# Performance work log

Measured on AMD Instinct MI355X. Metric: run time of the kernel, lower is better.

## Reference

```python
import jax, jax.numpy as jnp
import numpy as np

WS, SS, NH = 7, 3, 3  # window_size, shift_size, num_heads


def window_partition(x, ws):
    B, H, W, C = x.shape
    x = x.reshape(B, H // ws, ws, W // ws, ws, C)
    return jnp.transpose(x, (0, 1, 3, 2, 4, 5)).reshape(-1, ws, ws, C)


def window_reverse(w, ws, H, W):
    B = w.shape[0] // (H * W // ws // ws)
    x = w.reshape(B, H // ws, W // ws, ws, ws, -1)
    return jnp.transpose(x, (0, 1, 3, 2, 4, 5)).reshape(B, H, W, -1)


def layernorm(x, scale, bias, eps=1e-6):
    mu = x.mean(-1, keepdims=True)
    var = ((x - mu) ** 2).mean(-1, keepdims=True)
    return (x - mu) * jax.lax.rsqrt(var + eps) * scale + bias


def make_attn_mask(Hp, Wp, ws, ss):
    # static (trace-time) shifted-window mask, (nW, N, N)
    img = np.zeros((1, Hp, Wp, 1), np.float32)
    cnt = 0
    for h in (slice(0, -ws), slice(-ws, -ss), slice(-ss, None)):
        for w in (slice(0, -ws), slice(-ws, -ss), slice(-ss, None)):
            img[:, h, w, :] = cnt
            cnt += 1
    mw = img.reshape(1, Hp // ws, ws, Wp // ws, ws, 1).transpose(0, 1, 3, 2, 4, 5).reshape(-1, ws * ws)
    am = mw[:, None, :] - mw[:, :, None]
    return np.where(am != 0, -100.0, 0.0).astype(np.float32)


def setup_inputs() -> dict:
    key = jax.random.key(0)
    ks = jax.random.split(key, 8)
    B, H, W, C = 4, 56, 56, 96
    s = lambda k, shape: jax.random.normal(k, shape, jnp.float32) * 0.02
    return {
        'x': jax.random.normal(ks[0], (B, H * W, C), jnp.float32),
        'Hp': H, 'Wp': W,
        'norm1_scale': jnp.ones((C,), jnp.float32), 'norm1_bias': jnp.zeros((C,), jnp.float32),
        'qkv_w': s(ks[1], (C, 3 * C)), 'qkv_b': jnp.zeros((3 * C,), jnp.float32),
        'proj_w': s(ks[2], (C, C)), 'proj_b': jnp.zeros((C,), jnp.float32),
        'tb_ln1_scale': jnp.ones((C,), jnp.float32), 'tb_ln1_bias': jnp.zeros((C,), jnp.float32),
        'tb_qkv_w': s(ks[3], (C, 3 * C)), 'tb_qkv_b': jnp.zeros((3 * C,), jnp.float32),
        'tb_out_w': s(ks[4], (C, C)), 'tb_out_b': jnp.zeros((C,), jnp.float32),
        'tb_ln2_scale': jnp.ones((C,), jnp.float32), 'tb_ln2_bias': jnp.zeros((C,), jnp.float32),
        'tb_fc1_w': s(ks[5], (C, 4 * C)), 'tb_fc1_b': jnp.zeros((4 * C,), jnp.float32),
        'tb_fc2_w': s(ks[6], (4 * C, C)), 'tb_fc2_b': jnp.zeros((C,), jnp.float32),
    }


def reference(x, Hp, Wp, norm1_scale, norm1_bias, qkv_w, qkv_b, proj_w, proj_b,
              tb_ln1_scale, tb_ln1_bias, tb_qkv_w, tb_qkv_b, tb_out_w, tb_out_b,
              tb_ln2_scale, tb_ln2_bias, tb_fc1_w, tb_fc1_b, tb_fc2_w, tb_fc2_b):
    ws, ss, nh = WS, SS, NH
    B, L, C = x.shape
    H, W = int(Hp), int(Wp)
    hd = C // nh
    shortcut = x
    h = layernorm(x, norm1_scale, norm1_bias).reshape(B, H, W, C)
    pad_r = (ws - W % ws) % ws
    pad_b = (ws - H % ws) % ws
    h = jnp.pad(h, ((0, 0), (0, pad_b), (0, pad_r), (0, 0)))
    Hpad, Wpad = H + pad_b, W + pad_r
    shifted = jnp.roll(h, (-ss, -ss), (1, 2))
    attn_mask = jnp.asarray(make_attn_mask(Hpad, Wpad, ws, ss))  # (nW, N, N)
    xw = window_partition(shifted, ws).reshape(-1, ws * ws, C)  # (B*nW, N, C)
    Bw, N, _ = xw.shape
    qkv = (xw @ qkv_w + qkv_b).reshape(Bw, N, 3, nh, hd).transpose(2, 0, 3, 1, 4)
    q, k, v = qkv[0], qkv[1], qkv[2]
    attn = jnp.einsum('bhnd,bhmd->bhnm', q, k) * hd ** -0.5
    nW = attn_mask.shape[0]
    attn = attn.reshape(Bw // nW, nW, nh, N, N) + attn_mask[None, :, None]
    attn = jax.nn.softmax(attn.reshape(-1, nh, N, N), axis=-1)
    out = jnp.einsum('bhnm,bhmd->bhnd', attn, v).transpose(0, 2, 1, 3).reshape(Bw, N, C)
    out = out @ proj_w + proj_b
    out = window_reverse(out.reshape(-1, ws, ws, C), ws, Hpad, Wpad)
    out = jnp.roll(out, (ss, ss), (1, 2))[:, :H, :W, :].reshape(B, H * W, C)
    x = shortcut + out
    # trailing pre-LN transformer block: global MHSA + MLP
    y = layernorm(x, tb_ln1_scale, tb_ln1_bias)
    qkv2 = (y @ tb_qkv_w + tb_qkv_b).reshape(B, L, 3, nh, hd).transpose(2, 0, 3, 1, 4)
    q2, k2, v2 = qkv2[0], qkv2[1], qkv2[2]
    a2 = jax.nn.softmax(jnp.einsum('bhnd,bhmd->bhnm', q2, k2) * hd ** -0.5, axis=-1)
    ao = jnp.einsum('bhnm,bhmd->bhnd', a2, v2).transpose(0, 2, 1, 3).reshape(B, L, C)
    x = x + (ao @ tb_out_w + tb_out_b)
    z = layernorm(x, tb_ln2_scale, tb_ln2_bias)
    z = jax.nn.gelu(z @ tb_fc1_w + tb_fc1_b) @ tb_fc2_w + tb_fc2_b
    x = x + z
    return (x, H, W)
```

## Files before the change

kernel.cpp:

```cpp
#include <hip/hip_runtime.h>
#include <hip/hip_bf16.h>

#define CD 96
#define LROW 3136
#define QSCALE 0.17677669529663687f
#define LOG2E 1.4426950408889634f
#define MASKLOG2 -144.26950408889634f

using f32x4 = __attribute__((ext_vector_type(4))) float;
using bf8   = __attribute__((ext_vector_type(8))) short;

__device__ __forceinline__ short f2bf(float f) {
  union { float f; unsigned u; } v; v.f = f;
  unsigned r = v.u + 0x7fffu + ((v.u >> 16) & 1u);
  return (short)(r >> 16);
}
__device__ __forceinline__ float bf2f(unsigned short s) {
  return __uint_as_float((unsigned)s << 16);
}
__device__ __forceinline__ unsigned pack_bf2(float lo, float hi) {
  return (__float_as_uint(hi) & 0xffff0000u) | (__float_as_uint(lo) >> 16);
}
__device__ __forceinline__ unsigned pack_bf2r(float lo, float hi) {
  return ((unsigned)(unsigned short)f2bf(hi) << 16) | (unsigned short)f2bf(lo);
}
__device__ __forceinline__ float fast_exp2(float x) {
  return __builtin_amdgcn_exp2f(x);
}
__device__ __forceinline__ float gelu_f(float v) {
  float u = 0.7978845608028654f * (v + 0.044715f * v * v * v);
  float e = fast_exp2(u * 2.8853900817779268f);
  return v * e * __builtin_amdgcn_rcpf(e + 1.f);
}

#define GLOAD_LDS16(src, dst) \
  __builtin_amdgcn_global_load_lds((const __attribute__((address_space(1))) void*)(src), \
                                   (__attribute__((address_space(3))) void*)(dst), 16, 0, 0)

__global__ __launch_bounds__(256) void ln_kernel(const float* __restrict__ x,
                                                 const float* __restrict__ g,
                                                 const float* __restrict__ b,
                                                 short* __restrict__ out, int rows) {
  int slot = threadIdx.x >> 5, l32 = threadIdx.x & 31;
  int row = blockIdx.x * 8 + slot;
  if (row >= rows) return;
  const float* xr = x + (size_t)row * CD + l32 * 3;
  float a0 = xr[0], a1 = xr[1], a2 = xr[2];
  float s = a0 + a1 + a2;
#pragma unroll
  for (int off = 16; off >= 1; off >>= 1) s += __shfl_xor(s, off, 32);
  float mu = s * (1.f / 96.f);
  float d0 = a0 - mu, d1 = a1 - mu, d2 = a2 - mu;
  float q = d0 * d0 + d1 * d1 + d2 * d2;
#pragma unroll
  for (int off = 16; off >= 1; off >>= 1) q += __shfl_xor(q, off, 32);
  float rstd = rsqrtf(q * (1.f / 96.f) + 1e-6f);
  int c0 = l32 * 3;
  short* orow = out + (size_t)row * CD + c0;
  orow[0] = f2bf(d0 * rstd * g[c0] + b[c0]);
  orow[1] = f2bf(d1 * rstd * g[c0 + 1] + b[c0 + 1]);
  orow[2] = f2bf(d2 * rstd * g[c0 + 2] + b[c0 + 2]);
}

__global__ __launch_bounds__(256) void cvt_all_kernel(
    const float* __restrict__ qkv2_w, const float* __restrict__ out_w,
    const float* __restrict__ fc1_w, const float* __restrict__ fc2_w,
    const float* __restrict__ qkv_w, const float* __restrict__ proj_w,
    short* __restrict__ dst,
    const int* __restrict__ Hp, const int* __restrict__ Wp,
    float* __restrict__ tail_out) {
  int idx = blockIdx.x * 256 + threadIdx.x;
  if (idx == 0) {
    tail_out[0] = (float)Hp[0];
    tail_out[1] = (float)Wp[0];
  }
  if (idx >= 165888) return;
  const float* W; int K, N, off;
  if (idx < 30720)       { W = qkv2_w; K = 96;  N = 288; off = idx; }
  else if (idx < 43008)  { W = out_w;  K = 96;  N = 96;  off = idx - 30720; }
  else if (idx < 79872)  { W = fc1_w;  K = 96;  N = 384; off = idx - 43008; }
  else if (idx < 129024) { W = fc2_w;  K = 384; N = 96;  off = idx - 79872; }
  else if (idx < 156672) { W = qkv_w;  K = 96;  N = 288; off = idx - 129024; }
  else                   { W = proj_w; K = 96;  N = 96;  off = idx - 156672; }
  int nr = off / K, kk = off - nr * K;
  float v = (nr < N) ? W[(size_t)kk * N + nr] : 0.f;
  dst[idx] = f2bf(v);
}

__global__ __launch_bounds__(512) void win_attn_kernel(
    const short* __restrict__ hb_in, const float* __restrict__ xin,
    const short* __restrict__ wwin, const float* __restrict__ qkv_b,
    const short* __restrict__ wproj, const float* __restrict__ proj_b,
    const float* __restrict__ ln1s, const float* __restrict__ ln1b,
    float* __restrict__ x1, short* __restrict__ hb2) {
  __shared__ __align__(16) short Xs[64][104];
  __shared__ __align__(16) short Qs[3][64][40];
  __shared__ __align__(16) short Ks[3][64][40];
  __shared__ __align__(16) short Vt[3][32][72];
  __shared__ __align__(16) short Os[64][104];
  __shared__ __align__(16) short Ptw[8][16][72];
  __shared__ int cnt[64];
  __shared__ int gidx[49];

  int tid = threadIdx.x, lane = tid & 63, wid = tid >> 6;
  int lr = lane & 15, lg = lane >> 4;
  int b = blockIdx.x >> 6, w64 = blockIdx.x & 63;
  int wr = w64 >> 3, wc = w64 & 7;

  if (tid < 64) {
    if (tid < 49) {
      int i = tid / 7, j = tid % 7;
      int sh = wr * 7 + i, sw = wc * 7 + j;
      int hr = (sh < 49) ? 0 : ((sh < 53) ? 1 : 2);
      int wreg = (sw < 49) ? 0 : ((sw < 53) ? 1 : 2);
      cnt[tid] = hr * 3 + wreg;
      gidx[tid] = ((sh + 3) % 56) * 56 + ((sw + 3) % 56);
    } else {
      cnt[tid] = -1;
    }
  }
  __syncthreads();

  for (int c = tid; c < 768; c += 512) {
    int row = c / 12, cc = c % 12;
    uint4 v = {0u, 0u, 0u, 0u};
    if (row < 49) v = *reinterpret_cast<const uint4*>(hb_in + ((size_t)b * LROW + gidx[row]) * 96 + cc * 8);
    *reinterpret_cast<uint4*>(&Xs[row][cc * 8]) = v;
  }
  __syncthreads();

  for (int nt = wid; nt < 18; nt += 8) {
    f32x4 acc[4];
#pragma unroll
    for (int mi = 0; mi < 4; ++mi) acc[mi] = (f32x4){0.f, 0.f, 0.f, 0.f};
#pragma unroll
    for (int kc = 0; kc < 3; ++kc) {
      bf8 bfr = *reinterpret_cast<const bf8*>(wwin + (size_t)(nt * 16 + lr) * 96 + kc * 32 + lg * 8);
#pragma unroll
      for (int mi = 0; mi < 4; ++mi) {
        bf8 afr = *reinterpret_cast<const bf8*>(&Xs[mi * 16 + lr][kc * 32 + lg * 8]);
        acc[mi] = __builtin_amdgcn_mfma_f32_16x16x32_bf16(afr, bfr, acc[mi], 0, 0, 0);
      }
    }
    int n = nt * 16 + lr;
    int sec = n / 96, within = n % 96;
    int hh = within >> 5, dd = within & 31;
    float bias = qkv_b[n];
#pragma unroll
    for (int mi = 0; mi < 4; ++mi)
#pragma unroll
      for (int r = 0; r < 4; ++r) {
        int mrow = mi * 16 + lg * 4 + r;
        float v = acc[mi][r] + bias;
        if (sec == 0)      Qs[hh][mrow][dd] = f2bf(v * (QSCALE * LOG2E));
        else if (sec == 1) Ks[hh][mrow][dd] = f2bf(v);
        else               Vt[hh][dd][mrow] = f2bf(v);
      }
  }
  __syncthreads();

  int cntkv[16];
#pragma unroll
  for (int t = 0; t < 4; ++t)
#pragma unroll
    for (int r = 0; r < 4; ++r) cntkv[t * 4 + r] = cnt[t * 16 + lg * 4 + r];

  for (int p = wid; p < 12; p += 8) {
    int h = p >> 2, qt = p & 3;
    bf8 qf = *reinterpret_cast<const bf8*>(&Qs[h][qt * 16 + lr][lg * 8]);
    int cq = cnt[qt * 16 + lr];
    f32x4 z = {0.f, 0.f, 0.f, 0.f};
    f32x4 St[4];
    __builtin_amdgcn_s_setprio(1);
#pragma unroll
    for (int t = 0; t < 4; ++t) {
      bf8 kf = *reinterpret_cast<const bf8*>(&Ks[h][t * 16 + lr][lg * 8]);
      St[t] = __builtin_amdgcn_mfma_f32_16x16x32_bf16(kf, qf, z, 0, 0, 0);
    }
    __builtin_amdgcn_s_setprio(0);
    float pr[4];
#pragma unroll
    for (int t = 0; t < 4; ++t) {
      float p0 = fast_exp2(St[t][0] + ((cq == cntkv[t * 4 + 0]) ? 0.f : MASKLOG2));
      float p1 = fast_exp2(St[t][1] + ((cq == cntkv[t * 4 + 1]) ? 0.f : MASKLOG2));
      float p2 = fast_exp2(St[t][2] + ((cq == cntkv[t * 4 + 2]) ? 0.f : MASKLOG2));
      float p3 = fast_exp2(St[t][3] + ((cq == cntkv[t * 4 + 3]) ? 0.f : MASKLOG2));
      St[t][0] = p0; St[t][1] = p1; St[t][2] = p2; St[t][3] = p3;
      pr[t] = (p0 + p1) + (p2 + p3);
    }
    float rs = (pr[0] + pr[1]) + (pr[2] + pr[3]);
    rs += __shfl_xor(rs, 16);
    rs += __shfl_xor(rs, 32);
    float inv = 1.f / rs;
#pragma unroll
    for (int t = 0; t < 4; ++t) {
      uint2 w;
      w.x = pack_bf2(St[t][0], St[t][1]);
      w.y = pack_bf2(St[t][2], St[t][3]);
      *reinterpret_cast<uint2*>(&Ptw[wid][lr][t * 16 + lg * 4]) = w;
    }
    f32x4 O0 = {0.f, 0.f, 0.f, 0.f}, O1 = {0.f, 0.f, 0.f, 0.f};
    __builtin_amdgcn_s_setprio(1);
#pragma unroll
    for (int c = 0; c < 2; ++c) {
      bf8 pbf = *reinterpret_cast<const bf8*>(&Ptw[wid][lr][c * 32 + lg * 8]);
      bf8 v0 = *reinterpret_cast<const bf8*>(&Vt[h][lr][c * 32 + lg * 8]);
      bf8 v1 = *reinterpret_cast<const bf8*>(&Vt[h][16 + lr][c * 32 + lg * 8]);
      O0 = __builtin_amdgcn_mfma_f32_16x16x32_bf16(v0, pbf, O0, 0, 0, 0);
      O1 = __builtin_amdgcn_mfma_f32_16x16x32_bf16(v1, pbf, O1, 0, 0, 0);
    }
    __builtin_amdgcn_s_setprio(0);
#pragma unroll
    for (int r = 0; r < 4; ++r) {
      Os[qt * 16 + lr][h * 32 + lg * 4 + r] = f2bf(O0[r] * inv);
      Os[qt * 16 + lr][h * 32 + 16 + lg * 4 + r] = f2bf(O1[r] * inv);
    }
  }
  __syncthreads();

  if (wid < 4) {
    int mt = wid;
    f32x4 acc[6];
#pragma unroll
    for (int nt = 0; nt < 6; ++nt) acc[nt] = (f32x4){0.f, 0.f, 0.f, 0.f};
#pragma unroll
    for (int kc = 0; kc < 3; ++kc) {
      bf8 afr = *reinterpret_cast<const bf8*>(&Os[mt * 16 + lr][kc * 32 + lg * 8]);
#pragma unroll
      for (int nt = 0; nt < 6; ++nt) {
        bf8 bfr = *reinterpret_cast<const bf8*>(wproj + (size_t)(nt * 16 + lr) * 96 + kc * 32 + lg * 8);
        acc[nt] = __builtin_amdgcn_mfma_f32_16x16x32_bf16(afr, bfr, acc[nt], 0, 0, 0);
      }
    }
    float pbv[6], gv[6], bv[6];
#pragma unroll
    for (int nt = 0; nt < 6; ++nt) {
      int col = nt * 16 + lr;
      pbv[nt] = proj_b[col];
      gv[nt] = ln1s[col];
      bv[nt] = ln1b[col];
    }
#pragma unroll
    for (int r = 0; r < 4; ++r) {
      int q = mt * 16 + lg * 4 + r;
      if (q >= 49) continue;
      size_t rb = ((size_t)b * LROW + gidx[q]) * CD;
      float v[6];
#pragma unroll
      for (int nt = 0; nt < 6; ++nt)
        v[nt] = acc[nt][r] + pbv[nt] + xin[rb + nt * 16 + lr];
      float s = ((v[0] + v[1]) + (v[2] + v[3])) + (v[4] + v[5]);
      s += __shfl_xor(s, 1); s += __shfl_xor(s, 2);
      s += __shfl_xor(s, 4); s += __shfl_xor(s, 8);
      float mu = s * (1.f / 96.f);
      float d[6];
      float qs = 0.f;
#pragma unroll
      for (int nt = 0; nt < 6; ++nt) { d[nt] = v[nt] - mu; qs += d[nt] * d[nt]; }
      qs += __shfl_xor(qs, 1); qs += __shfl_xor(qs, 2);
      qs += __shfl_xor(qs, 4); qs += __shfl_xor(qs, 8);
      float rstd = rsqrtf(qs * (1.f / 96.f) + 1e-6f);
#pragma unroll
      for (int nt = 0; nt < 6; ++nt) {
        x1[rb + nt * 16 + lr] = v[nt];
        hb2[rb + nt * 16 + lr] = f2bf(d[nt] * rstd * gv[nt] + bv[nt]);
      }
    }
  }
}

__global__ __launch_bounds__(256) void qkv_mfma_kernel(
    const short* __restrict__ A, const short* __restrict__ Bt,
    const float* __restrict__ bias,
    short* __restrict__ qb, short* __restrict__ kb, short* __restrict__ vtb) {
  __shared__ __align__(16) short As[2][128 * 32];
  __shared__ __align__(16) short Bs[2][64 * 32];
  int tid = threadIdx.x, lane = tid & 63, wid = tid >> 6;
  int lr = lane & 15, lg = lane >> 4;
  int m0 = blockIdx.x * 128, n0 = blockIdx.y * 64;
  const int K = 96;

  f32x4 acc[2][4];
#pragma unroll
  for (int i = 0; i < 2; ++i)
#pragma unroll
    for (int j = 0; j < 4; ++j) acc[i][j] = (f32x4){0.f, 0.f, 0.f, 0.f};

  auto stage = [&](int bf, int ks) {
    int k0 = ks * 32;
#pragma unroll
    for (int p = 0; p < 2; ++p) {
      int idx = tid + p * 256;
      GLOAD_LDS16(A + (size_t)(m0 + (idx >> 2)) * K + k0 + (idx & 3) * 8,
                  &As[bf][idx * 8]);
    }
    GLOAD_LDS16(Bt + (size_t)(n0 + (tid >> 2)) * K + k0 + (tid & 3) * 8,
                &Bs[bf][tid * 8]);
  };

  stage(0, 0);
  __syncthreads();
  int buf = 0;
  for (int ks = 0; ks < 3; ++ks) {
    if (ks + 1 < 3) stage(buf ^ 1, ks + 1);
    bf8 bfr[4], afr[2];
#pragma unroll
    for (int ni = 0; ni < 4; ++ni)
      bfr[ni] = *reinterpret_cast<const bf8*>(&Bs[buf][(ni * 16 + lr) * 32 + lg * 8]);
#pragma unroll
    for (int mi = 0; mi < 2; ++mi)
      afr[mi] = *reinterpret_cast<const bf8*>(&As[buf][(wid * 32 + mi * 16 + lr) * 32 + lg * 8]);
    __builtin_amdgcn_s_setprio(1);
#pragma unroll
    for (int mi = 0; mi < 2; ++mi)
#pragma unroll
      for (int ni = 0; ni < 4; ++ni)
        acc[mi][ni] = __builtin_amdgcn_mfma_f32_16x16x32_bf16(afr[mi], bfr[ni], acc[mi][ni], 0, 0, 0);
    __builtin_amdgcn_s_setprio(0);
    __syncthreads();
    buf ^= 1;
  }

#pragma unroll
  for (int mi = 0; mi < 2; ++mi)
#pragma unroll
    for (int ni = 0; ni < 4; ++ni)
#pragma unroll
      for (int r = 0; r < 4; ++r) {
        int mrow = m0 + wid * 32 + mi * 16 + lg * 4 + r;
        int n = n0 + ni * 16 + lr;
        if (n < 288) {
          float v = acc[mi][ni][r] + bias[n];
          int sec = n / 96, within = n % 96;
          int hh = within >> 5, dd = within & 31;
          int bb = mrow / LROW, nn = mrow - bb * LROW;
          size_t bh = (size_t)bb * 3 + hh;
          if (sec == 0)      qb[(bh * LROW + nn) * 32 + dd] = f2bf(v * (QSCALE * LOG2E));
          else if (sec == 1) kb[(bh * LROW + nn) * 32 + dd] = f2bf(v);
          else               vtb[((bh * 49 + (nn >> 6)) * 32 + dd) * 64 + (nn & 63)] = f2bf(v);
        }
      }
}

__global__ __launch_bounds__(128) void flash_mfma_kernel(
    const short* __restrict__ qb, const short* __restrict__ kb,
    const short* __restrict__ vtb,
    short* __restrict__ pOb, float* __restrict__ pl) {
  __shared__ __align__(16) short Pt[2][2][16][72];
  int tid = threadIdx.x, lane = tid & 63, wid = tid >> 6;
  int lr = lane & 15, lg = lane >> 4;
  int bh = blockIdx.y, s = blockIdx.z;
  int q0 = blockIdx.x * 64 + wid * 32;
  const short* qbb = qb + (size_t)bh * LROW * 32;
  const short* kbase = kb + (size_t)bh * LROW * 32 + lr * 32 + lg * 8;
  const short* vbase = vtb + (size_t)bh * 49 * 2048 + lr * 64 + lg * 8;

  bf8 qf0 = *reinterpret_cast<const bf8*>(qbb + (size_t)(q0 + lr) * 32 + lg * 8);
  bf8 qf1 = *reinterpret_cast<const bf8*>(qbb + (size_t)(q0 + 16 + lr) * 32 + lg * 8);

  const bf8 onesf = {16256, 16256, 16256, 16256, 16256, 16256, 16256, 16256};

  f32x4 O00 = {0.f,0.f,0.f,0.f}, O01 = {0.f,0.f,0.f,0.f};
  f32x4 O10 = {0.f,0.f,0.f,0.f}, O11 = {0.f,0.f,0.f,0.f};
  f32x4 La0 = {0.f,0.f,0.f,0.f}, La1 = {0.f,0.f,0.f,0.f};

  const int tbl[7] = {0, 9, 17, 25, 33, 41, 49};
  int t0 = tbl[s], t1 = tbl[s + 1];

  bf8 kA[4], vA[4], kB[4], vB[4];

  auto loadt = [&](bf8 (&Kf)[4], bf8 (&Vf)[4], int kt) {
    const short* kp = kbase + (size_t)kt * 2048;
#pragma unroll
    for (int t = 0; t < 4; ++t) Kf[t] = *reinterpret_cast<const bf8*>(kp + t * 512);
    const short* vp = vbase + (size_t)kt * 2048;
#pragma unroll
    for (int c = 0; c < 2; ++c) {
      Vf[c]     = *reinterpret_cast<const bf8*>(vp + c * 32);
      Vf[2 + c] = *reinterpret_cast<const bf8*>(vp + 1024 + c * 32);
    }
  };

  auto body = [&](bf8 (&Kf)[4], bf8 (&Vf)[4]) {
    f32x4 z = {0.f, 0.f, 0.f, 0.f};
#pragma unroll
    for (int g = 0; g < 2; ++g) {
      bf8 qf = g ? qf1 : qf0;
      f32x4 St[4];
      __builtin_amdgcn_s_setprio(1);
#pragma unroll
      for (int t = 0; t < 4; ++t)
        St[t] = __builtin_amdgcn_mfma_f32_16x16x32_bf16(Kf[t], qf, z, 0, 0, 0);
      __builtin_amdgcn_s_setprio(0);
#pragma unroll
      for (int t = 0; t < 4; ++t) {
        float p0 = fast_exp2(St[t][0]);
        float p1 = fast_exp2(St[t][1]);
        float p2 = fast_exp2(St[t][2]);
        float p3 = fast_exp2(St[t][3]);
        uint2 w;
        w.x = pack_bf2(p0, p1);
        w.y = pack_bf2(p2, p3);
        *reinterpret_cast<uint2*>(&Pt[wid][g][lr][t * 16 + lg * 4]) = w;
      }
    }
    __builtin_amdgcn_s_setprio(1);
#pragma unroll
    for (int g = 0; g < 2; ++g) {
      f32x4& Oh0 = g ? O10 : O00;
      f32x4& Oh1 = g ? O11 : O01;
      f32x4& La  = g ? La1 : La0;
#pragma unroll
      for (int c = 0; c < 2; ++c) {
        bf8 pbf = *reinterpret_cast<const bf8*>(&Pt[wid][g][lr][c * 32 + lg * 8]);
        Oh0 = __builtin_amdgcn_mfma_f32_16x16x32_bf16(Vf[c], pbf, Oh0, 0, 0, 0);
        Oh1 = __builtin_amdgcn_mfma_f32_16x16x32_bf16(Vf[2 + c], pbf, Oh1, 0, 0, 0);
        La  = __builtin_amdgcn_mfma_f32_16x16x32_bf16(onesf, pbf, La, 0, 0, 0);
      }
    }
    __builtin_amdgcn_s_setprio(0);
  };

  loadt(kA, vA, t0);
  int kt = t0;
  for (; kt + 2 <= t1 - 1; kt += 2) {
    loadt(kB, vB, kt + 1);
    body(kA, vA);
    loadt(kA, vA, kt + 2);
    body(kB, vB);
  }
  if (kt < t1 - 1) {
    loadt(kB, vB, kt + 1);
    body(kA, vA);
    body(kB, vB);
  } else {
    body(kA, vA);
  }

  size_t rbase = (size_t)(s * 12 + bh) * LROW;
  size_t r0 = (rbase + q0 + lr) * 32;
  size_t r1 = (rbase + q0 + 16 + lr) * 32;
  uint2 w;
  w.x = pack_bf2r(O00[0], O00[1]); w.y = pack_bf2r(O00[2], O00[3]);
  *reinterpret_cast<uint2*>(&pOb[r0 + lg * 4]) = w;
  w.x = pack_bf2r(O01[0], O01[1]); w.y = pack_bf2r(O01[2], O01[3]);
  *reinterpret_cast<uint2*>(&pOb[r0 + 16 + lg * 4]) = w;
  w.x = pack_bf2r(O10[0], O10[1]); w.y = pack_bf2r(O10[2], O10[3]);
  *reinterpret_cast<uint2*>(&pOb[r1 + lg * 4]) = w;
  w.x = pack_bf2r(O11[0], O11[1]); w.y = pack_bf2r(O11[2], O11[3]);
  *reinterpret_cast<uint2*>(&pOb[r1 + 16 + lg * 4]) = w;
  if (lg == 0) {
    pl[rbase + q0 + lr] = La0[0];
    pl[rbase + q0 + 16 + lr] = La1[0];
  }
}

__global__ __launch_bounds__(256) void gemm_out_merge_ln_kernel(
    const short* __restrict__ pOb, const float* __restrict__ pl,
    const short* __restrict__ Bt,
    const float* __restrict__ bias, const float* __restrict__ res,
    const float* __restrict__ g2, const float* __restrict__ b2,
    float* __restrict__ x2, short* __restrict__ hb3) {
  __shared__ __align__(16) short As[128][104];
  __shared__ __align__(16) short Bs[2][96 * 32];
  int tid = threadIdx.x, lane = tid & 63, wid = tid >> 6;
  int lr = lane & 15, lg = lane >> 4;
  int m0 = blockIdx.x * 128;
  const int K = 96;
  const int NR = 12 * LROW;

  for (int pi = tid; pi < 384; pi += 256) {
    int rloc = pi / 3, h = pi % 3;
    int grow = m0 + rloc;
    int bb = grow / LROW, q = grow - bb * LROW;
    size_t pbase = ((size_t)(bb * 3 + h)) * LROW + q;
    float l = 0.f;
#pragma unroll
    for (int s = 0; s < 6; ++s) l += pl[(size_t)s * NR + pbase];
    float invl = 1.f / l;
    float o[32];
#pragma unroll
    for (int d = 0; d < 32; ++d) o[d] = 0.f;
#pragma unroll
    for (int s = 0; s < 6; ++s) {
      const uint4* p4 = reinterpret_cast<const uint4*>(pOb + ((size_t)s * NR + pbase) * 32);
#pragma unroll
      for (int u = 0; u < 4; ++u) {
        uint4 v = p4[u];
        unsigned wd0 = v.x, wd1 = v.y, wd2 = v.z, wd3 = v.w;
        o[u*8+0] += __uint_as_float(wd0 << 16);
        o[u*8+1] += __uint_as_float(wd0 & 0xffff0000u);
        o[u*8+2] += __uint_as_float(wd1 << 16);
        o[u*8+3] += __uint_as_float(wd1 & 0xffff0000u);
        o[u*8+4] += __uint_as_float(wd2 << 16);
        o[u*8+5] += __uint_as_float(wd2 & 0xffff0000u);
        o[u*8+6] += __uint_as_float(wd3 << 16);
        o[u*8+7] += __uint_as_float(wd3 & 0xffff0000u);
      }
    }
    short* dst = &As[rloc][h * 32];
#pragma unroll
    for (int u2 = 0; u2 < 4; ++u2) {
      uint4 w;
      w.x = pack_bf2r(o[u2*8+0]*invl, o[u2*8+1]*invl);
      w.y = pack_bf2r(o[u2*8+2]*invl, o[u2*8+3]*invl);
      w.z = pack_bf2r(o[u2*8+4]*invl, o[u2*8+5]*invl);
      w.w = pack_bf2r(o[u2*8+6]*invl, o[u2*8+7]*invl);
      *reinterpret_cast<uint4*>(dst + u2 * 8) = w;
    }
  }

  f32x4 acc[2][6];
#pragma unroll
  for (int i = 0; i < 2; ++i)
#pragma unroll
    for (int j = 0; j < 6; ++j) acc[i][j] = (f32x4){0.f, 0.f, 0.f, 0.f};

  auto stageB = [&](int bf, int ks) {
    int k0 = ks * 32;
    for (int l = tid; l < 384; l += 256) {
      GLOAD_LDS16(Bt + (size_t)(l >> 2) * K + k0 + (l & 3) * 8,
                  &Bs[bf][l * 8]);
    }
  };

  stageB(0, 0);
  __syncthreads();
  int buf = 0;
  for (int ks = 0; ks < 3; ++ks) {
    if (ks + 1 < 3) stageB(buf ^ 1, ks + 1);
    bf8 bfr[6], afr[2];
#pragma unroll
    for (int ni = 0; ni < 6; ++ni)
      bfr[ni] = *reinterpret_cast<const bf8*>(&Bs[buf][(ni * 16 + lr) * 32 + lg * 8]);
#pragma unroll
    for (int mi = 0; mi < 2; ++mi)
      afr[mi] = *reinterpret_cast<const bf8*>(&As[wid * 32 + mi * 16 + lr][ks * 32 + lg * 8]);
    __builtin_amdgcn_s_setprio(1);
#pragma unroll
    for (int mi = 0; mi < 2; ++mi)
#pragma unroll
      for (int ni = 0; ni < 6; ++ni)
        acc[mi][ni] = __builtin_amdgcn_mfma_f32_16x16x32_bf16(afr[mi], bfr[ni], acc[mi][ni], 0, 0, 0);
    __builtin_amdgcn_s_setprio(0);
    __syncthreads();
    buf ^= 1;
  }

  float bb[6], gv[6], bv[6];
#pragma unroll
  for (int ni = 0; ni < 6; ++ni) {
    int col = ni * 16 + lr;
    bb[ni] = bias[col];
    gv[ni] = g2[col];
    bv[ni] = b2[col];
  }
#pragma unroll
  for (int mi = 0; mi < 2; ++mi)
#pragma unroll
    for (int r = 0; r < 4; ++r) {
      int row = m0 + wid * 32 + mi * 16 + lg * 4 + r;
      size_t rb = (size_t)row * CD;
      float v[6];
#pragma unroll
      for (int ni = 0; ni < 6; ++ni)
        v[ni] = acc[mi][ni][r] + bb[ni] + res[rb + ni * 16 + lr];
      float s = ((v[0] + v[1]) + (v[2] + v[3])) + (v[4] + v[5]);
      s += __shfl_xor(s, 1); s += __shfl_xor(s, 2);
      s += __shfl_xor(s, 4); s += __shfl_xor(s, 8);
      float mu = s * (1.f / 96.f);
      float d[6];
      float qs = 0.f;
#pragma unroll
      for (int ni = 0; ni < 6; ++ni) { d[ni] = v[ni] - mu; qs += d[ni] * d[ni]; }
      qs += __shfl_xor(qs, 1); qs += __shfl_xor(qs, 2);
      qs += __shfl_xor(qs, 4); qs += __shfl_xor(qs, 8);
      float rstd = rsqrtf(qs * (1.f / 96.f) + 1e-6f);
#pragma unroll
      for (int ni = 0; ni < 6; ++ni) {
        x2[rb + ni * 16 + lr] = v[ni];
        hb3[rb + ni * 16 + lr] = f2bf(d[ni] * rstd * gv[ni] + bv[ni]);
      }
    }
}

__global__ __launch_bounds__(256) void mlp_kernel(
    const short* __restrict__ hb3, const short* __restrict__ wfc1,
    const float* __restrict__ fc1_b, const short* __restrict__ wfc2,
    const float* __restrict__ fc2_b, const float* __restrict__ resid,
    float* __restrict__ outx) {
  __shared__ __align__(16) short Ah[64][104];
  __shared__ __align__(16) short T[64][392];
  int tid = threadIdx.x, lane = tid & 63, wid = tid >> 6;
  int lr = lane & 15, lg = lane >> 4;
  int m0 = blockIdx.x * 64;

  for (int i = tid; i < 768; i += 256) {
    int row = i / 12, c8 = i % 12;
    uint4 v = *reinterpret_cast<const uint4*>(hb3 + (size_t)(m0 + row) * 96 + c8 * 8);
    *reinterpret_cast<uint4*>(&Ah[row][c8 * 8]) = v;
  }
  __syncthreads();

  {
    f32x4 acc[4][6];
#pragma unroll
    for (int i = 0; i < 4; ++i)
#pragma unroll
      for (int j = 0; j < 6; ++j) acc[i][j] = (f32x4){0.f, 0.f, 0.f, 0.f};
#pragma unroll
    for (int kc = 0; kc < 3; ++kc) {
      bf8 bfr[6], afr[4];
#pragma unroll
      for (int nt = 0; nt < 6; ++nt)
        bfr[nt] = *reinterpret_cast<const bf8*>(wfc1 + (size_t)(wid * 96 + nt * 16 + lr) * 96 + kc * 32 + lg * 8);
#pragma unroll
      for (int mi = 0; mi < 4; ++mi)
        afr[mi] = *reinterpret_cast<const bf8*>(&Ah[mi * 16 + lr][kc * 32 + lg * 8]);
      __builtin_amdgcn_s_setprio(1);
#pragma unroll
      for (int mi = 0; mi < 4; ++mi)
#pragma unroll
        for (int nt = 0; nt < 6; ++nt)
          acc[mi][nt] = __builtin_amdgcn_mfma_f32_16x16x32_bf16(afr[mi], bfr[nt], acc[mi][nt], 0, 0, 0);
      __builtin_amdgcn_s_setprio(0);
    }
#pragma unroll
    for (int nt = 0; nt < 6; ++nt) {
      float b1 = fc1_b[wid * 96 + nt * 16 + lr];
      int col = wid * 96 + nt * 16 + lr;
#pragma unroll
      for (int mi = 0; mi < 4; ++mi)
#pragma unroll
        for (int r = 0; r < 4; ++r)
          T[mi * 16 + lg * 4 + r][col] = f2bf(gelu_f(acc[mi][nt][r] + b1));
    }
  }
  __syncthreads();

  {
    f32x4 a2[6];
#pragma unroll
    for (int j = 0; j < 6; ++j) a2[j] = (f32x4){0.f, 0.f, 0.f, 0.f};
#pragma unroll
    for (int kc = 0; kc < 12; ++kc) {
      bf8 afr2 = *reinterpret_cast<const bf8*>(&T[wid * 16 + lr][kc * 32 + lg * 8]);
      bf8 bfr2[6];
#pragma unroll
      for (int nt = 0; nt < 6; ++nt)
        bfr2[nt] = *reinterpret_cast<const bf8*>(wfc2 + (size_t)(nt * 16 + lr) * 384 + kc * 32 + lg * 8);
      __builtin_amdgcn_s_setprio(1);
#pragma unroll
      for (int nt = 0; nt < 6; ++nt)
        a2[nt] = __builtin_amdgcn_mfma_f32_16x16x32_bf16(afr2, bfr2[nt], a2[nt], 0, 0, 0);
      __builtin_amdgcn_s_setprio(0);
    }
#pragma unroll
    for (int nt = 0; nt < 6; ++nt) {
      float b2v = fc2_b[nt * 16 + lr];
#pragma unroll
      for (int r = 0; r < 4; ++r) {
        int row = m0 + wid * 16 + lg * 4 + r;
        size_t idx = (size_t)row * CD + nt * 16 + lr;
        outx[idx] = a2[nt][r] + b2v + resid[idx];
      }
    }
  }
}

extern "C" void kernel_launch(void* const* d_in, const int* in_sizes, int n_in,
                              void* d_out, int out_size, void* d_ws, size_t ws_size,
                              hipStream_t stream) {
  const float* x      = (const float*)d_in[0];
  const int*   Hp     = (const int*)d_in[1];
  const int*   Wp     = (const int*)d_in[2];
  const float* n1s    = (const float*)d_in[3];
  const float* n1b    = (const float*)d_in[4];
  const float* qkv_w  = (const float*)d_in[5];
  const float* qkv_b  = (const float*)d_in[6];
  const float* proj_w = (const float*)d_in[7];
  const float* proj_b = (const float*)d_in[8];
  const float* ln1s   = (const float*)d_in[9];
  const float* ln1b   = (const float*)d_in[10];
  const float* qkv2_w = (const float*)d_in[11];
  const float* qkv2_b = (const float*)d_in[12];
  const float* out_w  = (const float*)d_in[13];
  const float* out_b  = (const float*)d_in[14];
  const float* ln2s   = (const float*)d_in[15];
  const float* ln2b   = (const float*)d_in[16];
  const float* fc1_w  = (const float*)d_in[17];
  const float* fc1_b  = (const float*)d_in[18];
  const float* fc2_w  = (const float*)d_in[19];
  const float* fc2_b  = (const float*)d_in[20];

  float* wsf = (float*)d_ws;
  const size_t U = (size_t)4 * LROW * CD;
  float* x1   = wsf;
  short* hb   = (short*)(wsf + 2 * U);
  short* qb   = (short*)(wsf + 4 * U + U / 2);
  short* kb   = qb + U;
  short* vtb  = kb + U;
  short* wall = (short*)(wsf + 6 * U);
  short* wqkv = wall;
  short* wout = wqkv + 320 * 96;
  short* wfc1 = wout + 128 * 96;
  short* wfc2 = wfc1 + 384 * 96;
  short* wwin = wfc2 + 128 * 384;
  short* wproj = wwin + 288 * 96;
  short* hb2  = (short*)(wsf + 6 * U + 82944);
  short* pOb  = (short*)(wsf + U);
  float* pl   = wsf + 4 * U;
  float* x2f  = (float*)qb;
  short* hb3  = vtb;
  float* outx = (float*)d_out;

  const int M = 4 * LROW;

  cvt_all_kernel<<<(165888 + 255) / 256, 256, 0, stream>>>(
      qkv2_w, out_w, fc1_w, fc2_w, qkv_w, proj_w, wall, Hp, Wp, outx + U);

  ln_kernel<<<M / 8, 256, 0, stream>>>(x, n1s, n1b, hb, M);
  win_attn_kernel<<<256, 512, 0, stream>>>(hb, x, wwin, qkv_b, wproj, proj_b,
                                           ln1s, ln1b, x1, hb2);
  qkv_mfma_kernel<<<dim3(M / 128, 5), 256, 0, stream>>>(hb2, wqkv, qkv2_b, qb, kb, vtb);
  flash_mfma_kernel<<<dim3(49, 12, 6), 128, 0, stream>>>(qb, kb, vtb, pOb, pl);
  gemm_out_merge_ln_kernel<<<M / 128, 256, 0, stream>>>(pOb, pl, wout, out_b, x1,
                                                        ln2s, ln2b, x2f, hb3);
  mlp_kernel<<<M / 64, 256, 0, stream>>>(hb3, wfc1, fc1_b, wfc2, fc2_b, x2f, outx);
}
```

Before: 114.3 us.

## Fuse norm1 LayerNorm into window attention and swizzle flash block order

Removes the standalone LayerNorm kernel and computes norm1 directly inside the window-attention kernel from the fp32 input, writing bf16 rows into shared memory and zeroing the padding rows. This drops one launch and the bf16 intermediate round trip through global memory. Separately, the flash attention grid is flattened to 1D and remapped with an XCD-style swizzle (flat&7)*441 so that consecutive blocks on the same XCD share head/split data for L2 locality. In exchange, the window kernel does the extra LN work serially within its 256 blocks.

```diff
diff --git a/kernel.cpp b/kernel.cpp
--- a/kernel.cpp
+++ b/kernel.cpp
@@ -36,31 +36,6 @@
 #define GLOAD_LDS16(src, dst) \
   __builtin_amdgcn_global_load_lds((const __attribute__((address_space(1))) void*)(src), \
                                    (__attribute__((address_space(3))) void*)(dst), 16, 0, 0)
-
-__global__ __launch_bounds__(256) void ln_kernel(const float* __restrict__ x,
-                                                 const float* __restrict__ g,
-                                                 const float* __restrict__ b,
-                                                 short* __restrict__ out, int rows) {
-  int slot = threadIdx.x >> 5, l32 = threadIdx.x & 31;
-  int row = blockIdx.x * 8 + slot;
-  if (row >= rows) return;
-  const float* xr = x + (size_t)row * CD + l32 * 3;
-  float a0 = xr[0], a1 = xr[1], a2 = xr[2];
-  float s = a0 + a1 + a2;
-#pragma unroll
-  for (int off = 16; off >= 1; off >>= 1) s += __shfl_xor(s, off, 32);
-  float mu = s * (1.f / 96.f);
-  float d0 = a0 - mu, d1 = a1 - mu, d2 = a2 - mu;
-  float q = d0 * d0 + d1 * d1 + d2 * d2;
-#pragma unroll
-  for (int off = 16; off >= 1; off >>= 1) q += __shfl_xor(q, off, 32);
-  float rstd = rsqrtf(q * (1.f / 96.f) + 1e-6f);
-  int c0 = l32 * 3;
-  short* orow = out + (size_t)row * CD + c0;
-  orow[0] = f2bf(d0 * rstd * g[c0] + b[c0]);
-  orow[1] = f2bf(d1 * rstd * g[c0 + 1] + b[c0 + 1]);
-  orow[2] = f2bf(d2 * rstd * g[c0 + 2] + b[c0 + 2]);
-}
 
 __global__ __launch_bounds__(256) void cvt_all_kernel(
     const float* __restrict__ qkv2_w, const float* __restrict__ out_w,
@@ -88,7 +63,8 @@
 }
 
 __global__ __launch_bounds__(512) void win_attn_kernel(
-    const short* __restrict__ hb_in, const float* __restrict__ xin,
+    const float* __restrict__ xin,
+    const float* __restrict__ n1s, const float* __restrict__ n1b,
     const short* __restrict__ wwin, const float* __restrict__ qkv_b,
     const short* __restrict__ wproj, const float* __restrict__ proj_b,
     const float* __restrict__ ln1s, const float* __restrict__ ln1b,
@@ -121,11 +97,31 @@
   }
   __syncthreads();
 
-  for (int c = tid; c < 768; c += 512) {
-    int row = c / 12, cc = c % 12;
-    uint4 v = {0u, 0u, 0u, 0u};
-    if (row < 49) v = *reinterpret_cast<const uint4*>(hb_in + ((size_t)b * LROW + gidx[row]) * 96 + cc * 8);
-    *reinterpret_cast<uint4*>(&Xs[row][cc * 8]) = v;
+  for (int i = tid; i < 180; i += 512) {
+    int row = 49 + i / 12, c8 = i % 12;
+    uint4 z4 = {0u, 0u, 0u, 0u};
+    *reinterpret_cast<uint4*>(&Xs[row][c8 * 8]) = z4;
+  }
+  {
+    int grp = tid >> 5, l32 = tid & 31;
+    int c0 = l32 * 3;
+    for (int row = grp; row < 49; row += 16) {
+      const float* xr = xin + ((size_t)b * LROW + gidx[row]) * CD + c0;
+      float a0 = xr[0], a1 = xr[1], a2 = xr[2];
+      float s = a0 + a1 + a2;
+#pragma unroll
+      for (int off = 16; off >= 1; off >>= 1) s += __shfl_xor(s, off, 32);
+      float mu = s * (1.f / 96.f);
+      float d0 = a0 - mu, d1 = a1 - mu, d2 = a2 - mu;
+      float q = d0 * d0 + d1 * d1 + d2 * d2;
+#pragma unroll
+      for (int off = 16; off >= 1; off >>= 1) q += __shfl_xor(q, off, 32);
+      float rstd = rsqrtf(q * (1.f / 96.f) + 1e-6f);
+      short* orow = &Xs[row][c0];
+      orow[0] = f2bf(d0 * rstd * n1s[c0] + n1b[c0]);
+      orow[1] = f2bf(d1 * rstd * n1s[c0 + 1] + n1b[c0 + 1]);
+      orow[2] = f2bf(d2 * rstd * n1s[c0 + 2] + n1b[c0 + 2]);
+    }
   }
   __syncthreads();
 
@@ -349,8 +345,14 @@
   __shared__ __align__(16) short Pt[2][2][16][72];
   int tid = threadIdx.x, lane = tid & 63, wid = tid >> 6;
   int lr = lane & 15, lg = lane >> 4;
-  int bh = blockIdx.y, s = blockIdx.z;
-  int q0 = blockIdx.x * 64 + wid * 32;
+
+  int flat = blockIdx.x;
+  int swz = (flat & 7) * 441 + (flat >> 3);
+  int qt = swz % 49;
+  int yz = swz / 49;
+  int bh = yz % 12, s = yz / 12;
+
+  int q0 = qt * 64 + wid * 32;
   const short* qbb = qb + (size_t)bh * LROW * 32;
   const short* kbase = kb + (size_t)bh * LROW * 32 + lr * 32 + lg * 8;
   const short* vbase = vtb + (size_t)bh * 49 * 2048 + lr * 64 + lg * 8;
@@ -696,7 +698,6 @@
   float* wsf = (float*)d_ws;
   const size_t U = (size_t)4 * LROW * CD;
   float* x1   = wsf;
-  short* hb   = (short*)(wsf + 2 * U);
   short* qb   = (short*)(wsf + 4 * U + U / 2);
   short* kb   = qb + U;
   short* vtb  = kb + U;
@@ -719,11 +720,10 @@
   cvt_all_kernel<<<(165888 + 255) / 256, 256, 0, stream>>>(
       qkv2_w, out_w, fc1_w, fc2_w, qkv_w, proj_w, wall, Hp, Wp, outx + U);
 
-  ln_kernel<<<M / 8, 256, 0, stream>>>(x, n1s, n1b, hb, M);
-  win_attn_kernel<<<256, 512, 0, stream>>>(hb, x, wwin, qkv_b, wproj, proj_b,
+  win_attn_kernel<<<256, 512, 0, stream>>>(x, n1s, n1b, wwin, qkv_b, wproj, proj_b,
                                            ln1s, ln1b, x1, hb2);
   qkv_mfma_kernel<<<dim3(M / 128, 5), 256, 0, stream>>>(hb2, wqkv, qkv2_b, qb, kb, vtb);
-  flash_mfma_kernel<<<dim3(49, 12, 6), 128, 0, stream>>>(qb, kb, vtb, pOb, pl);
+  flash_mfma_kernel<<<3528, 128, 0, stream>>>(qb, kb, vtb, pOb, pl);
   gemm_out_merge_ln_kernel<<<M / 128, 256, 0, stream>>>(pOb, pl, wout, out_b, x1,
                                                         ln2s, ln2b, x2f, hb3);
   mlp_kernel<<<M / 64, 256, 0, stream>>>(hb3, wfc1, fc1_b, wfc2, fc2_b, x2f, outx);
```

New measurement: 118.2 us. +3.4%, slower.
